# Kernel optimization log

Measured on AMD Instinct MI355X. Metric: run time of the kernel, lower is better.

Reference implementation:

```python
import jax, jax.numpy as jnp
import numpy as np

HEAD_NUM = 16

def setup_inputs() -> dict:
    key = jax.random.key(0)
    ks = jax.random.split(key, 5)
    B, N, D = 2, 2048, 1024
    x = jax.random.normal(ks[0], (B, N, D), dtype=jnp.float32)
    scale = 0.02
    W_q = jax.random.normal(ks[1], (D, D), dtype=jnp.float32) * scale
    W_k = jax.random.normal(ks[2], (D, D), dtype=jnp.float32) * scale
    W_v = jax.random.normal(ks[3], (D, D), dtype=jnp.float32) * scale
    W_o = jax.random.normal(ks[4], (D, D), dtype=jnp.float32) * scale
    return {"x": x, "W_q": W_q, "W_k": W_k, "W_v": W_v, "W_o": W_o}

def reference(x, W_q, W_k, W_v, W_o):
    B, N, D = x.shape
    H = HEAD_NUM
    hd = D // H  # head_dim
    inv_sqrt_hd = 1.0 / np.sqrt(hd).astype(np.float32)

    def split_head(t):
        # einops 'b n (d h) -> b h n d' : head index is the INNER factor
        return t.reshape(B, N, hd, H).transpose(0, 3, 1, 2)  # [B,H,N,hd]

    # nn.Linear(bias=False): y = x @ W.T
    Q = split_head(x @ W_q.T)
    K = split_head(x @ W_k.T)
    V = split_head(x @ W_v.T)

    scores = jnp.einsum('bhnd,bhmd->bhnm', Q, K) * inv_sqrt_hd  # [B,H,N,N]
    attn = jax.nn.softmax(scores, axis=-1)
    heads = jnp.einsum('bhnm,bhmd->bhnd', attn, V)  # [B,H,N,hd]

    # einops 'b h n d -> b n (h d)' : head index is the OUTER factor here
    concat = heads.transpose(0, 2, 1, 3).reshape(B, N, D)
    return concat @ W_o.T
```

## Files before the change

### kernel.cpp

```cpp
#include <hip/hip_runtime.h>
#include <hip/hip_bf16.h>

typedef __bf16 bf16_t;
typedef __attribute__((ext_vector_type(8))) __bf16 bf16x8;
typedef __attribute__((ext_vector_type(4))) __bf16 bf16x4;
typedef __attribute__((ext_vector_type(4))) float f32x4;
typedef __attribute__((ext_vector_type(16))) float f32x16;

#define MFMA16(A,B,C) __builtin_amdgcn_mfma_f32_16x16x32_bf16((A),(B),(C),0,0,0)
#define MFMA32(A,B,C) __builtin_amdgcn_mfma_f32_32x32x16_bf16((A),(B),(C),0,0,0)

#define BATCH 2
#define SEQ 2048
#define DMODEL 1024
#define NHEAD 16
#define HDIM 64
#define MROWS (BATCH * SEQ)

__device__ __forceinline__ void async16(const bf16_t* g, bf16_t* l) {
    __builtin_amdgcn_global_load_lds(
        (const __attribute__((address_space(1))) unsigned int*)g,
        (__attribute__((address_space(3))) unsigned int*)l, 16, 0, 0);
}

__device__ __forceinline__ bf16x8 ldsA32(const bf16_t* base, int row, int chunk) {
    return *(const bf16x8*)&base[row * 32 + ((chunk ^ ((row >> 1) & 3)) << 3)];
}

__device__ __forceinline__ unsigned pk(float a, float b) {
    union { unsigned u; bf16_t h[2]; } t;
    t.h[0] = (bf16_t)a;
    t.h[1] = (bf16_t)b;
    return t.u;
}

__device__ __forceinline__ void plane32_swap(unsigned& d, unsigned& s) {
    asm("v_permlane32_swap_b32 %0, %1" : "+v"(d), "+v"(s));
}

__device__ __forceinline__ void sm_pack(const f32x16& st, float* rsp, bf16x8* pf) {
    float pexp[16];
#pragma unroll
    for (int r = 0; r < 16; ++r)
        pexp[r] = __builtin_amdgcn_exp2f(st[r]);
    rsp[0] += pexp[0] + pexp[4] + pexp[8] + pexp[12];
    rsp[1] += pexp[1] + pexp[5] + pexp[9] + pexp[13];
    rsp[2] += pexp[2] + pexp[6] + pexp[10] + pexp[14];
    rsp[3] += pexp[3] + pexp[7] + pexp[11] + pexp[15];
#pragma unroll
    for (int s1 = 0; s1 < 2; ++s1) {
        unsigned lo01 = pk(pexp[8 * s1 + 0], pexp[8 * s1 + 1]);
        unsigned lo23 = pk(pexp[8 * s1 + 2], pexp[8 * s1 + 3]);
        unsigned hi01 = pk(pexp[8 * s1 + 4], pexp[8 * s1 + 5]);
        unsigned hi23 = pk(pexp[8 * s1 + 6], pexp[8 * s1 + 7]);
        plane32_swap(lo01, hi01);
        plane32_swap(lo23, hi23);
        union { bf16x8 v; unsigned u[4]; } outv;
        outv.u[0] = lo01;
        outv.u[1] = lo23;
        outv.u[2] = hi01;
        outv.u[3] = hi23;
        pf[s1] = outv.v;
    }
}

__global__ void split_kernel(const float* __restrict__ x, const float* __restrict__ Wq,
                             const float* __restrict__ Wk, const float* __restrict__ Wv,
                             const float* __restrict__ Wo, bf16_t* __restrict__ xh,
                             bf16_t* __restrict__ wh) {
    int blk = blockIdx.x;
    if (blk < 4096) {
        int i = blk * 256 + threadIdx.x;
        f32x4 v = ((const f32x4*)x)[i];
        bf16x4 h;
#pragma unroll
        for (int c = 0; c < 4; ++c) h[c] = (bf16_t)v[c];
        ((bf16x4*)xh)[i] = h;
        return;
    }
    int e = blk - 4096;
    int z = e >> 10;
    int i = (e & 1023) * 256 + threadIdx.x;
    const float* src = (z == 0) ? Wq : (z == 1) ? Wk : (z == 2) ? Wv : Wo;
    const float scale = (z == 0) ? 0.125f * 1.44269504088896f : 1.0f;
    int row = i >> 8, col4 = i & 255;
    int r_src;
    if (z < 3) {
        int h = row >> 6, d = row & 63;
        r_src = 16 * d + h;
    } else {
        r_src = row;
    }
    f32x4 v = ((const f32x4*)src)[r_src * 256 + col4];
    bf16x4 h4;
#pragma unroll
    for (int c = 0; c < 4; ++c) h4[c] = (bf16_t)(v[c] * scale);
    ((bf16x4*)(wh + (size_t)z * DMODEL * DMODEL))[i] = h4;
}

__global__ __launch_bounds__(256)
void gemm_qkv_kernel(const bf16_t* __restrict__ Ah, const bf16_t* __restrict__ Bh0,
                     bf16_t* __restrict__ Coh0, bf16_t* __restrict__ Vt,
                     int M, int Nn, int Kk) {
    __shared__ __align__(16) bf16_t smem[2][8192];

    const int id = blockIdx.x;
    const int xcd = id & 7;
    const int t = id >> 3;
    const int n0i = t & 7;
    const int u = t >> 3;
    const int z = u >> 2;
    const int m0g = u & 3;
    const int m0 = (m0g * 8 + xcd) * 128;
    const int n0 = n0i * 128;

    const bf16_t* Bh = Bh0 + (size_t)z * Nn * Kk;
    const int tid = threadIdx.x;
    const int wave = tid >> 6, lane = tid & 63, lq = lane >> 4, ln = lane & 15;
    const int wr = wave >> 1, wc = wave & 1;

    const bf16_t* g_ptr[4];
    int l_off[4];
#pragma unroll
    for (int q = 0; q < 4; ++q) {
        int e = wave * 4 + q;
        int a = e >> 3, uu = e & 7;
        int C = uu * 64 + lane;
        int r = C >> 2, p = C & 3;
        int c = p ^ ((r >> 1) & 3);
        g_ptr[q] = (a == 0 ? Ah + (size_t)(m0 + r) * Kk
                           : Bh + (size_t)(n0 + r) * Kk) + c * 8;
        l_off[q] = a * 4096 + uu * 512;
    }

    f32x4 acc[4][4] = {};

#pragma unroll
    for (int q = 0; q < 4; ++q)
        async16(g_ptr[q], &smem[0][l_off[q]]);

    const int NIT = Kk / 32;
    for (int j = 0; j < NIT; ++j) {
        __syncthreads();
        if (j + 1 < NIT) {
#pragma unroll
            for (int q = 0; q < 4; ++q)
                async16(g_ptr[q] + (j + 1) * 32, &smem[(j + 1) & 1][l_off[q]]);
        }
        const bf16_t* cur = smem[j & 1];

        bf16x8 ah[4], bh[4];
#pragma unroll
        for (int tt = 0; tt < 4; ++tt) {
            ah[tt] = ldsA32(cur, wr * 64 + tt * 16 + ln, lq);
            bh[tt] = ldsA32(cur + 4096, wc * 64 + tt * 16 + ln, lq);
        }
#pragma unroll
        for (int tm = 0; tm < 4; ++tm)
#pragma unroll
            for (int tn = 0; tn < 4; ++tn)
                acc[tm][tn] = MFMA16(ah[tm], bh[tn], acc[tm][tn]);
    }

    if (z != 2) {
#pragma unroll
        for (int tm = 0; tm < 4; ++tm)
#pragma unroll
            for (int tn = 0; tn < 4; ++tn)
#pragma unroll
                for (int p = 0; p < 4; ++p) {
                    int gm = m0 + wr * 64 + tm * 16 + lq * 4 + p;
                    int gn = n0 + wc * 64 + tn * 16 + ln;
                    Coh0[(size_t)z * M * Nn + (size_t)gm * Nn + gn] =
                        (bf16_t)acc[tm][tn][p];
                }
    } else {
#pragma unroll
        for (int tm = 0; tm < 4; ++tm)
#pragma unroll
            for (int tn = 0; tn < 4; ++tn) {
                int gn = n0 + wc * 64 + tn * 16 + ln;
                int hh = gn >> 6, dd = gn & 63;
                int gm0 = m0 + wr * 64 + tm * 16 + lq * 4;
                int bb = gm0 >> 11, nn = gm0 & 2047;
                bf16x4 v4;
#pragma unroll
                for (int p = 0; p < 4; ++p) v4[p] = (bf16_t)acc[tm][tn][p];
                *(bf16x4*)&Vt[(((size_t)(bb * NHEAD + hh)) * HDIM + dd) * SEQ + nn] = v4;
            }
    }
}

__global__ __launch_bounds__(256)
void gemm_out_kernel(const bf16_t* __restrict__ Ah, const bf16_t* __restrict__ Bh,
                     float* __restrict__ Cf, int M, int Nn, int Kk) {
    __shared__ __align__(16) bf16_t smem[2][6144];

    const int id = blockIdx.x;
    const int xcd = id & 7;
    const int t = id >> 3;
    const int n0i = t & 7;
    const int m0g = t >> 3;
    const int m0 = (m0g * 8 + xcd) * 64;
    const int n0 = n0i * 128;

    const int tid = threadIdx.x;
    const int wave = tid >> 6, lane = tid & 63, lq = lane >> 4, ln = lane & 15;
    const int wr = wave >> 1, wc = wave & 1;

    const bf16_t* g_ptr[3];
    int l_off[3];
#pragma unroll
    for (int q = 0; q < 3; ++q) {
        int e = wave * 3 + q;
        const bf16_t* arr;
        int u, rowbase, lb;
        if (e < 4) { arr = Ah; u = e;     rowbase = m0; lb = 0; }
        else       { arr = Bh; u = e - 4; rowbase = n0; lb = 2048; }
        int r = u * 16 + (lane >> 2), p = lane & 3;
        int c = p ^ ((r >> 1) & 3);
        g_ptr[q] = arr + (size_t)(rowbase + r) * Kk + c * 8;
        l_off[q] = lb + u * 512;
    }

    f32x4 acc[2][4] = {};

#pragma unroll
    for (int q = 0; q < 3; ++q)
        async16(g_ptr[q], &smem[0][l_off[q]]);

    const int NIT = Kk / 32;
    for (int j = 0; j < NIT; ++j) {
        __syncthreads();
        if (j + 1 < NIT) {
#pragma unroll
            for (int q = 0; q < 3; ++q)
                async16(g_ptr[q] + (j + 1) * 32, &smem[(j + 1) & 1][l_off[q]]);
        }
        const bf16_t* cur = smem[j & 1];

        bf16x8 ah[2], bh[4];
#pragma unroll
        for (int tt = 0; tt < 2; ++tt)
            ah[tt] = ldsA32(cur, wr * 32 + tt * 16 + ln, lq);
#pragma unroll
        for (int tt = 0; tt < 4; ++tt)
            bh[tt] = ldsA32(cur + 2048, wc * 64 + tt * 16 + ln, lq);
#pragma unroll
        for (int tm = 0; tm < 2; ++tm)
#pragma unroll
            for (int tn = 0; tn < 4; ++tn)
                acc[tm][tn] = MFMA16(ah[tm], bh[tn], acc[tm][tn]);
    }

#pragma unroll
    for (int tm = 0; tm < 2; ++tm)
#pragma unroll
        for (int tn = 0; tn < 4; ++tn)
#pragma unroll
            for (int p = 0; p < 4; ++p) {
                int gm = m0 + wr * 32 + tm * 16 + lq * 4 + p;
                int gn = n0 + wc * 64 + tn * 16 + ln;
                Cf[(size_t)gm * Nn + gn] = acc[tm][tn][p];
            }
}

__global__ __launch_bounds__(256, 2)
void attn_kernel(const bf16_t* __restrict__ Qh, const bf16_t* __restrict__ Kh,
                 const bf16_t* __restrict__ Vt, bf16_t* __restrict__ Ch) {
    __shared__ __align__(16) bf16_t smem[2][2][8192];

    const int id = blockIdx.x;
    const int bh = ((id >> 7) << 3) | (id & 7);
    const int qt = (id >> 3) & 15;
    const int b = bh >> 4, h = bh & 15;
    const int q0 = qt * 128;
    const int tid = threadIdx.x;
    const int g = tid >> 7;
    const int wv = (tid >> 6) & 1;
    const int lane = tid & 63;
    const int ln32 = lane & 31, hl = lane >> 5;

    bf16x8 qfh[2][4];
#pragma unroll
    for (int qs = 0; qs < 2; ++qs) {
        size_t qrow = ((size_t)(b * SEQ + q0 + wv * 64 + qs * 32 + ln32)) * DMODEL +
                      h * HDIM + hl * 8;
#pragma unroll
        for (int c = 0; c < 4; ++c)
            qfh[qs][c] = *(const bf16x8*)&Qh[qrow + c * 16];
    }

    const int xrow = ln32 * 64;
    int xc[4];
#pragma unroll
    for (int c = 0; c < 4; ++c)
        xc[c] = (((2 * c + hl) ^ (ln32 & 7)) << 3) + xrow;

    bf16_t* gsm = &smem[g][0][0];
    const bf16_t* gb;
    size_t ustep, jstep;
    int lb;
    {
        int r0 = lane >> 3, p = lane & 7;
        int c = p ^ (r0 & 7);
        if (wv == 0) {
            gb = Kh + ((size_t)(b * SEQ + g * 1024 + r0)) * DMODEL +
                 h * HDIM + c * 8;
            ustep = (size_t)8 * DMODEL;
            jstep = (size_t)64 * DMODEL;
            lb = 0;
        } else {
            gb = Vt + ((size_t)(bh * HDIM + r0)) * SEQ + g * 1024 + c * 8;
            ustep = (size_t)8 * SEQ;
            jstep = 64;
            lb = 4096;
        }
    }

    f32x16 o[2][2];
#pragma unroll
    for (int qs = 0; qs < 2; ++qs)
#pragma unroll
        for (int dt = 0; dt < 2; ++dt)
#pragma unroll
            for (int r = 0; r < 16; ++r) o[qs][dt][r] = 0.0f;
    float rsA[4] = {0.f, 0.f, 0.f, 0.f};
    float rsB[4] = {0.f, 0.f, 0.f, 0.f};

#pragma unroll
    for (int u = 0; u < 8; ++u)
        async16(gb + u * ustep, gsm + lb + u * 512);
    gb += jstep;

    for (int j = 0; j < 16; ++j) {
        __syncthreads();
        if (j < 15) {
#pragma unroll
            for (int u = 0; u < 8; ++u)
                async16(gb + u * ustep, gsm + ((j + 1) & 1) * 8192 + lb + u * 512);
            gb += jstep;
        }
        const bf16_t* Kc = gsm + (j & 1) * 8192;
        const bf16_t* Vc = Kc + 4096;

        bf16x8 pfA[4], pfB[4];
#pragma unroll
        for (int kt = 0; kt < 2; ++kt) {
            bf16x8 kh[4];
#pragma unroll
            for (int c = 0; c < 4; ++c)
                kh[c] = *(const bf16x8*)&Kc[kt * 2048 + xc[c]];
            f32x16 s0, s1;
#pragma unroll
            for (int r = 0; r < 16; ++r) { s0[r] = 0.0f; s1[r] = 0.0f; }
            __builtin_amdgcn_s_setprio(1);
#pragma unroll
            for (int c = 0; c < 4; ++c)
                s0 = MFMA32(kh[c], qfh[0][c], s0);
#pragma unroll
            for (int c = 0; c < 4; ++c)
                s1 = MFMA32(kh[c], qfh[1][c], s1);
            __builtin_amdgcn_s_setprio(0);
            sm_pack(s0, rsA, &pfA[kt * 2]);
            sm_pack(s1, rsB, &pfB[kt * 2]);
        }
        __builtin_amdgcn_s_setprio(1);
#pragma unroll
        for (int s = 0; s < 4; ++s) {
            bf16x8 va0 = *(const bf16x8*)&Vc[xc[s]];
            bf16x8 va1 = *(const bf16x8*)&Vc[2048 + xc[s]];
            o[0][0] = MFMA32(va0, pfA[s], o[0][0]);
            o[0][1] = MFMA32(va1, pfA[s], o[0][1]);
            o[1][0] = MFMA32(va0, pfB[s], o[1][0]);
            o[1][1] = MFMA32(va1, pfB[s], o[1][1]);
        }
        __builtin_amdgcn_s_setprio(0);
    }

    float rs[2];
    rs[0] = (rsA[0] + rsA[1]) + (rsA[2] + rsA[3]);
    rs[1] = (rsB[0] + rsB[1]) + (rsB[2] + rsB[3]);
#pragma unroll
    for (int qs = 0; qs < 2; ++qs)
        rs[qs] += __shfl_xor(rs[qs], 32);

    __syncthreads();
    float* cbuf = (float*)smem;
    float* rbuf = cbuf + 8192;
    if (g == 1) {
#pragma unroll
        for (int qs = 0; qs < 2; ++qs)
#pragma unroll
            for (int dt = 0; dt < 2; ++dt)
#pragma unroll
                for (int r = 0; r < 16; ++r) {
                    int d = dt * 32 + (r & 3) + 8 * (r >> 2) + 4 * hl;
                    cbuf[d * 128 + wv * 64 + qs * 32 + ln32] = o[qs][dt][r];
                }
        if (hl == 0) {
            rbuf[wv * 64 + ln32] = rs[0];
            rbuf[wv * 64 + 32 + ln32] = rs[1];
        }
    }
    __syncthreads();
    float inv[2] = {0.0f, 0.0f};
    if (g == 0) {
#pragma unroll
        for (int qs = 0; qs < 2; ++qs) {
#pragma unroll
            for (int dt = 0; dt < 2; ++dt)
#pragma unroll
                for (int r = 0; r < 16; ++r) {
                    int d = dt * 32 + (r & 3) + 8 * (r >> 2) + 4 * hl;
                    o[qs][dt][r] += cbuf[d * 128 + wv * 64 + qs * 32 + ln32];
                }
            inv[qs] = 1.0f / (rs[qs] + rbuf[wv * 64 + qs * 32 + ln32]);
        }
    }
    __syncthreads();
    float* fbuf = (float*)smem;
    if (g == 0) {
#pragma unroll
        for (int qs = 0; qs < 2; ++qs)
#pragma unroll
            for (int dh = 0; dh < 2; ++dh)
#pragma unroll
                for (int r = 0; r < 16; ++r) {
                    int d_loc = (r & 3) + 8 * (r >> 2) + 4 * hl;
                    fbuf[dh * 4224 + (wv * 2 + qs) * 1056 + ln32 * 33 + d_loc] =
                        o[qs][dh][r] * inv[qs];
                }
    }
    __syncthreads();
    {
        int gw = tid >> 6;
        int dh = gw >> 1, wpair = gw & 1;
#pragma unroll
        for (int ww = 0; ww < 2; ++ww) {
            int w = wpair * 2 + ww;
#pragma unroll
            for (int qq = 0; qq < 16; ++qq) {
                int qrow = hl * 16 + qq;
                float v = fbuf[dh * 4224 + w * 1056 + qrow * 33 + ln32];
                size_t gidx = ((size_t)(b * SEQ + q0 + w * 32 + qrow)) * DMODEL +
                              h * HDIM + dh * 32 + ln32;
                Ch[gidx] = (bf16_t)v;
            }
        }
    }
}

extern "C" void kernel_launch(void* const* d_in, const int* in_sizes, int n_in,
                              void* d_out, int out_size, void* d_ws, size_t ws_size,
                              hipStream_t stream) {
    const float* x  = (const float*)d_in[0];
    const float* Wq = (const float*)d_in[1];
    const float* Wk = (const float*)d_in[2];
    const float* Wv = (const float*)d_in[3];
    const float* Wo = (const float*)d_in[4];
    float* out = (float*)d_out;

    char* ws = (char*)d_ws;
    size_t off = 0;
    auto alloc = [&](size_t bytes) -> bf16_t* {
        bf16_t* p = (bf16_t*)(ws + off);
        off += (bytes + 255) & ~(size_t)255;
        return p;
    };
    const size_t XE = (size_t)MROWS * DMODEL;
    const size_t WE = (size_t)DMODEL * DMODEL;

    bf16_t* xh  = alloc(XE * 2);
    bf16_t* wh  = alloc(4 * WE * 2);
    bf16_t* qnh = alloc(3 * XE * 2);
    bf16_t* vth = alloc(XE * 2);
    bf16_t* ch  = alloc(XE * 2);
    (void)ws_size; (void)in_sizes; (void)n_in; (void)out_size;

    split_kernel<<<8192, 256, 0, stream>>>(x, Wq, Wk, Wv, Wo, xh, wh);

    gemm_qkv_kernel<<<768, 256, 0, stream>>>(xh, wh, qnh, vth, MROWS, DMODEL, DMODEL);

    attn_kernel<<<512, 256, 0, stream>>>(qnh, qnh + XE, vth, ch);

    gemm_out_kernel<<<512, 256, 0, stream>>>(ch, wh + 3 * WE, out, MROWS, DMODEL, DMODEL);
}
```

Before: 175.0 us.

## Use four-stage 32-key KV ring buffer with partial waitcnt in attention kernel

The attention inner loop is restructured from a two-buffer pipeline over 64-key tiles into a four-slot ring buffer over 32-key tiles, prefetching three tiles ahead. A raw s_barrier with an explicit vmcnt(8) wait replaces __syncthreads, so loads for later tiles can stay in flight across iterations. The V tile layout and swizzle are changed to match the 32-column tiles. The aim is to hide global-to-LDS latency better. The cost is more barriers per key and smaller MFMA batches per iteration. The final iterations reload tile 31 as a dummy load to keep the vmcnt accounting uniform.

```diff
diff --git a/kernel.cpp b/kernel.cpp
--- a/kernel.cpp
+++ b/kernel.cpp
@@ -268,7 +268,7 @@
 __global__ __launch_bounds__(256, 2)
 void attn_kernel(const bf16_t* __restrict__ Qh, const bf16_t* __restrict__ Kh,
                  const bf16_t* __restrict__ Vt, bf16_t* __restrict__ Ch) {
-    __shared__ __align__(16) bf16_t smem[2][2][8192];
+    __shared__ __align__(16) bf16_t smem[2][4][4096];
 
     const int id = blockIdx.x;
     const int bh = ((id >> 7) << 3) | (id & 7);
@@ -290,32 +290,35 @@
         for (int c = 0; c < 4; ++c)
             qfh[qs][c] = *(const bf16x8*)&Qh[qrow + c * 16];
     }
-
-    const int xrow = ln32 * 64;
-    int xc[4];
+    asm volatile("s_waitcnt vmcnt(0)" ::: "memory");
+
+    int xcK[4];
 #pragma unroll
     for (int c = 0; c < 4; ++c)
-        xc[c] = (((2 * c + hl) ^ (ln32 & 7)) << 3) + xrow;
+        xcK[c] = (((2 * c + hl) ^ (ln32 & 7)) << 3) + ln32 * 64;
+    int xcV[2];
+#pragma unroll
+    for (int s = 0; s < 2; ++s)
+        xcV[s] = (((2 * s + hl) ^ ((ln32 >> 1) & 3)) << 3) + ln32 * 32;
 
     bf16_t* gsm = &smem[g][0][0];
     const bf16_t* gb;
     size_t ustep, jstep;
     int lb;
-    {
+    if (wv == 0) {
         int r0 = lane >> 3, p = lane & 7;
         int c = p ^ (r0 & 7);
-        if (wv == 0) {
-            gb = Kh + ((size_t)(b * SEQ + g * 1024 + r0)) * DMODEL +
-                 h * HDIM + c * 8;
-            ustep = (size_t)8 * DMODEL;
-            jstep = (size_t)64 * DMODEL;
-            lb = 0;
-        } else {
-            gb = Vt + ((size_t)(bh * HDIM + r0)) * SEQ + g * 1024 + c * 8;
-            ustep = (size_t)8 * SEQ;
-            jstep = 64;
-            lb = 4096;
-        }
+        gb = Kh + ((size_t)(b * SEQ + g * 1024 + r0)) * DMODEL + h * HDIM + c * 8;
+        ustep = (size_t)8 * DMODEL;
+        jstep = (size_t)32 * DMODEL;
+        lb = 0;
+    } else {
+        int r0 = lane >> 2, p = lane & 3;
+        int c = p ^ ((r0 >> 1) & 3);
+        gb = Vt + ((size_t)(bh * HDIM + r0)) * SEQ + g * 1024 + c * 8;
+        ustep = (size_t)16 * SEQ;
+        jstep = 32;
+        lb = 2048;
     }
 
     f32x16 o[2][2];
@@ -329,47 +332,50 @@
     float rsB[4] = {0.f, 0.f, 0.f, 0.f};
 
 #pragma unroll
-    for (int u = 0; u < 8; ++u)
-        async16(gb + u * ustep, gsm + lb + u * 512);
-    gb += jstep;
-
-    for (int j = 0; j < 16; ++j) {
-        __syncthreads();
-        if (j < 15) {
-#pragma unroll
-            for (int u = 0; u < 8; ++u)
-                async16(gb + u * ustep, gsm + ((j + 1) & 1) * 8192 + lb + u * 512);
-            gb += jstep;
-        }
-        const bf16_t* Kc = gsm + (j & 1) * 8192;
-        const bf16_t* Vc = Kc + 4096;
-
-        bf16x8 pfA[4], pfB[4];
-#pragma unroll
-        for (int kt = 0; kt < 2; ++kt) {
-            bf16x8 kh[4];
-#pragma unroll
-            for (int c = 0; c < 4; ++c)
-                kh[c] = *(const bf16x8*)&Kc[kt * 2048 + xc[c]];
-            f32x16 s0, s1;
-#pragma unroll
-            for (int r = 0; r < 16; ++r) { s0[r] = 0.0f; s1[r] = 0.0f; }
-            __builtin_amdgcn_s_setprio(1);
-#pragma unroll
-            for (int c = 0; c < 4; ++c)
-                s0 = MFMA32(kh[c], qfh[0][c], s0);
-#pragma unroll
-            for (int c = 0; c < 4; ++c)
-                s1 = MFMA32(kh[c], qfh[1][c], s1);
-            __builtin_amdgcn_s_setprio(0);
-            sm_pack(s0, rsA, &pfA[kt * 2]);
-            sm_pack(s1, rsB, &pfB[kt * 2]);
-        }
+    for (int tix = 0; tix < 3; ++tix)
+#pragma unroll
+        for (int u = 0; u < 4; ++u)
+            async16(gb + (size_t)tix * jstep + u * ustep,
+                    gsm + tix * 4096 + lb + u * 512);
+
+    for (int j = 0; j < 32; ++j) {
+        asm volatile("s_waitcnt vmcnt(8)" ::: "memory");
+        __builtin_amdgcn_s_barrier();
+        __builtin_amdgcn_sched_barrier(0);
+        {
+            int idx = (j + 3 < 32) ? (j + 3) : 31;
+            const bf16_t* gsrc = gb + (size_t)idx * jstep;
+            bf16_t* ldst = gsm + (idx & 3) * 4096 + lb;
+#pragma unroll
+            for (int u = 0; u < 4; ++u)
+                async16(gsrc + u * ustep, ldst + u * 512);
+        }
+        const bf16_t* Kc = gsm + (j & 3) * 4096;
+        const bf16_t* Vc = Kc + 2048;
+
+        bf16x8 kh[4];
+#pragma unroll
+        for (int c = 0; c < 4; ++c)
+            kh[c] = *(const bf16x8*)&Kc[xcK[c]];
+        f32x16 s0, s1;
+#pragma unroll
+        for (int r = 0; r < 16; ++r) { s0[r] = 0.0f; s1[r] = 0.0f; }
         __builtin_amdgcn_s_setprio(1);
 #pragma unroll
-        for (int s = 0; s < 4; ++s) {
-            bf16x8 va0 = *(const bf16x8*)&Vc[xc[s]];
-            bf16x8 va1 = *(const bf16x8*)&Vc[2048 + xc[s]];
+        for (int c = 0; c < 4; ++c)
+            s0 = MFMA32(kh[c], qfh[0][c], s0);
+#pragma unroll
+        for (int c = 0; c < 4; ++c)
+            s1 = MFMA32(kh[c], qfh[1][c], s1);
+        __builtin_amdgcn_s_setprio(0);
+        bf16x8 pfA[2], pfB[2];
+        sm_pack(s0, rsA, pfA);
+        sm_pack(s1, rsB, pfB);
+        __builtin_amdgcn_s_setprio(1);
+#pragma unroll
+        for (int s = 0; s < 2; ++s) {
+            bf16x8 va0 = *(const bf16x8*)&Vc[xcV[s]];
+            bf16x8 va1 = *(const bf16x8*)&Vc[1024 + xcV[s]];
             o[0][0] = MFMA32(va0, pfA[s], o[0][0]);
             o[0][1] = MFMA32(va1, pfA[s], o[0][1]);
             o[1][0] = MFMA32(va0, pfB[s], o[1][0]);
```

Result: no change. 177.5 us (+1.4%).

## Double attention query tile to 256 rows per 512-thread block

Applied to the files above, without the earlier changes.

The attention kernel now uses 512-thread blocks, with 4 waves per key half each covering 64 query rows, so a block handles 256 queries and the grid drops from 512 to 256 blocks. Each K/V tile staged in shared memory is reused by twice as many query rows, which halves K/V global traffic, and the async load work is spread across 4 waves per group. The cross-group reduction and output staging are split into per-head-dim-half passes so they fit the same shared memory, at the cost of extra barriers. Occupancy drops to one block per CU, and on 256 CUs the grid is now a single wave, which may hurt latency hiding.

```diff
diff --git a/kernel.cpp b/kernel.cpp
--- a/kernel.cpp
+++ b/kernel.cpp
@@ -265,19 +265,19 @@
             }
 }
 
-__global__ __launch_bounds__(256, 2)
+__global__ __launch_bounds__(512, 1)
 void attn_kernel(const bf16_t* __restrict__ Qh, const bf16_t* __restrict__ Kh,
                  const bf16_t* __restrict__ Vt, bf16_t* __restrict__ Ch) {
     __shared__ __align__(16) bf16_t smem[2][2][8192];
 
     const int id = blockIdx.x;
-    const int bh = ((id >> 7) << 3) | (id & 7);
-    const int qt = (id >> 3) & 15;
+    const int bh = ((id >> 6) << 3) | (id & 7);
+    const int qt = (id >> 3) & 7;
     const int b = bh >> 4, h = bh & 15;
-    const int q0 = qt * 128;
+    const int q0 = qt * 256;
     const int tid = threadIdx.x;
-    const int g = tid >> 7;
-    const int wv = (tid >> 6) & 1;
+    const int g = tid >> 8;
+    const int wv = (tid >> 6) & 3;
     const int lane = tid & 63;
     const int ln32 = lane & 31, hl = lane >> 5;
 
@@ -298,23 +298,24 @@
         xc[c] = (((2 * c + hl) ^ (ln32 & 7)) << 3) + xrow;
 
     bf16_t* gsm = &smem[g][0][0];
-    const bf16_t* gb;
-    size_t ustep, jstep;
-    int lb;
-    {
-        int r0 = lane >> 3, p = lane & 7;
-        int c = p ^ (r0 & 7);
-        if (wv == 0) {
-            gb = Kh + ((size_t)(b * SEQ + g * 1024 + r0)) * DMODEL +
-                 h * HDIM + c * 8;
-            ustep = (size_t)8 * DMODEL;
-            jstep = (size_t)64 * DMODEL;
-            lb = 0;
+    const bf16_t* g_cur[4];
+    int l_off[4];
+    size_t g_step[4];
+#pragma unroll
+    for (int q = 0; q < 4; ++q) {
+        int e = wv * 4 + q;
+        int a = e >> 3, u = e & 7;
+        int r = u * 8 + (lane >> 3), p = lane & 7;
+        int c = p ^ (r & 7);
+        if (a == 0) {
+            g_cur[q] = Kh + ((size_t)(b * SEQ + g * 1024 + r)) * DMODEL +
+                       h * HDIM + c * 8;
+            l_off[q] = u * 512;
+            g_step[q] = (size_t)64 * DMODEL;
         } else {
-            gb = Vt + ((size_t)(bh * HDIM + r0)) * SEQ + g * 1024 + c * 8;
-            ustep = (size_t)8 * SEQ;
-            jstep = 64;
-            lb = 4096;
+            g_cur[q] = Vt + ((size_t)(bh * HDIM + r)) * SEQ + g * 1024 + c * 8;
+            l_off[q] = 4096 + u * 512;
+            g_step[q] = 64;
         }
     }
 
@@ -329,17 +330,19 @@
     float rsB[4] = {0.f, 0.f, 0.f, 0.f};
 
 #pragma unroll
-    for (int u = 0; u < 8; ++u)
-        async16(gb + u * ustep, gsm + lb + u * 512);
-    gb += jstep;
+    for (int q = 0; q < 4; ++q) {
+        async16(g_cur[q], gsm + l_off[q]);
+        g_cur[q] += g_step[q];
+    }
 
     for (int j = 0; j < 16; ++j) {
         __syncthreads();
         if (j < 15) {
 #pragma unroll
-            for (int u = 0; u < 8; ++u)
-                async16(gb + u * ustep, gsm + ((j + 1) & 1) * 8192 + lb + u * 512);
-            gb += jstep;
+            for (int q = 0; q < 4; ++q) {
+                async16(g_cur[q], gsm + ((j + 1) & 1) * 8192 + l_off[q]);
+                g_cur[q] += g_step[q];
+            }
         }
         const bf16_t* Kc = gsm + (j & 1) * 8192;
         const bf16_t* Vc = Kc + 4096;
@@ -388,66 +391,65 @@
     __syncthreads();
     float* cbuf = (float*)smem;
     float* rbuf = cbuf + 8192;
-    if (g == 1) {
-#pragma unroll
-        for (int qs = 0; qs < 2; ++qs)
-#pragma unroll
-            for (int dt = 0; dt < 2; ++dt)
+#pragma unroll
+    for (int dt = 0; dt < 2; ++dt) {
+        if (g == 1) {
+#pragma unroll
+            for (int qs = 0; qs < 2; ++qs)
 #pragma unroll
                 for (int r = 0; r < 16; ++r) {
-                    int d = dt * 32 + (r & 3) + 8 * (r >> 2) + 4 * hl;
-                    cbuf[d * 128 + wv * 64 + qs * 32 + ln32] = o[qs][dt][r];
+                    int d = (r & 3) + 8 * (r >> 2) + 4 * hl;
+                    cbuf[d * 256 + wv * 64 + qs * 32 + ln32] = o[qs][dt][r];
                 }
-        if (hl == 0) {
-            rbuf[wv * 64 + ln32] = rs[0];
-            rbuf[wv * 64 + 32 + ln32] = rs[1];
-        }
-    }
-    __syncthreads();
-    float inv[2] = {0.0f, 0.0f};
-    if (g == 0) {
-#pragma unroll
-        for (int qs = 0; qs < 2; ++qs) {
-#pragma unroll
-            for (int dt = 0; dt < 2; ++dt)
+            if (dt == 0 && hl == 0) {
+                rbuf[wv * 64 + ln32] = rs[0];
+                rbuf[wv * 64 + 32 + ln32] = rs[1];
+            }
+        }
+        __syncthreads();
+        if (g == 0) {
+#pragma unroll
+            for (int qs = 0; qs < 2; ++qs) {
 #pragma unroll
                 for (int r = 0; r < 16; ++r) {
-                    int d = dt * 32 + (r & 3) + 8 * (r >> 2) + 4 * hl;
-                    o[qs][dt][r] += cbuf[d * 128 + wv * 64 + qs * 32 + ln32];
+                    int d = (r & 3) + 8 * (r >> 2) + 4 * hl;
+                    o[qs][dt][r] += cbuf[d * 256 + wv * 64 + qs * 32 + ln32];
                 }
-            inv[qs] = 1.0f / (rs[qs] + rbuf[wv * 64 + qs * 32 + ln32]);
-        }
-    }
-    __syncthreads();
+                if (dt == 0) rs[qs] += rbuf[wv * 64 + qs * 32 + ln32];
+            }
+        }
+        __syncthreads();
+    }
+    float inv[2];
+    inv[0] = (g == 0) ? 1.0f / rs[0] : 0.0f;
+    inv[1] = (g == 0) ? 1.0f / rs[1] : 0.0f;
+
     float* fbuf = (float*)smem;
-    if (g == 0) {
-#pragma unroll
-        for (int qs = 0; qs < 2; ++qs)
-#pragma unroll
-            for (int dh = 0; dh < 2; ++dh)
+#pragma unroll
+    for (int dh = 0; dh < 2; ++dh) {
+        if (g == 0) {
+#pragma unroll
+            for (int qs = 0; qs < 2; ++qs)
 #pragma unroll
                 for (int r = 0; r < 16; ++r) {
                     int d_loc = (r & 3) + 8 * (r >> 2) + 4 * hl;
-                    fbuf[dh * 4224 + (wv * 2 + qs) * 1056 + ln32 * 33 + d_loc] =
+                    fbuf[(wv * 64 + qs * 32 + ln32) * 33 + d_loc] =
                         o[qs][dh][r] * inv[qs];
                 }
-    }
-    __syncthreads();
-    {
-        int gw = tid >> 6;
-        int dh = gw >> 1, wpair = gw & 1;
-#pragma unroll
-        for (int ww = 0; ww < 2; ++ww) {
-            int w = wpair * 2 + ww;
+        }
+        __syncthreads();
+        {
+            int gw = tid >> 6;
 #pragma unroll
             for (int qq = 0; qq < 16; ++qq) {
-                int qrow = hl * 16 + qq;
-                float v = fbuf[dh * 4224 + w * 1056 + qrow * 33 + ln32];
-                size_t gidx = ((size_t)(b * SEQ + q0 + w * 32 + qrow)) * DMODEL +
+                int qrow = gw * 32 + hl * 16 + qq;
+                float v = fbuf[qrow * 33 + ln32];
+                size_t gidx = ((size_t)(b * SEQ + q0 + qrow)) * DMODEL +
                               h * HDIM + dh * 32 + ln32;
                 Ch[gidx] = (bf16_t)v;
             }
         }
+        __syncthreads();
     }
 }
 
@@ -482,7 +484,7 @@
 
     gemm_qkv_kernel<<<768, 256, 0, stream>>>(xh, wh, qnh, vth, MROWS, DMODEL, DMODEL);
 
-    attn_kernel<<<512, 256, 0, stream>>>(qnh, qnh + XE, vth, ch);
+    attn_kernel<<<256, 512, 0, stream>>>(qnh, qnh + XE, vth, ch);
 
     gemm_out_kernel<<<512, 256, 0, stream>>>(ch, wh + 3 * WE, out, MROWS, DMODEL, DMODEL);
 }
```

Measured after the change: 172.3 us. Within noise of the previous version (-1.6%).
